# Optimization experiments

Measured on AMD Instinct MI355X. Metric: run time of the kernel, lower is better.

## Reference

```python
import jax, jax.numpy as jnp
import numpy as np

B, T, L, H = 16, 16, 512, 768


def setup_inputs() -> dict:
    key = jax.random.key(0)
    k1, k2, k3, k4, k5, k6 = jax.random.split(key, 6)
    hn = jax.random.normal(k1, (B, L, H), dtype=jnp.float32)
    decoder_out = jax.random.normal(k2, (B, L, H), dtype=jnp.float32)
    W1 = jax.random.normal(k3, (H, H), dtype=jnp.float32) * (1.0 / np.sqrt(H))
    W2 = jax.random.normal(k4, (H, H), dtype=jnp.float32) * (1.0 / np.sqrt(H))
    V = jax.random.normal(k5, (H,), dtype=jnp.float32) * (1.0 / np.sqrt(H))
    # Ragged, consistent pointer indices: T monotone segment starts per sample,
    # gold boundary Yindex[b,t] in [Xindex[b,t], L).
    step = L // T  # 32
    Xindex = jnp.broadcast_to(jnp.arange(T, dtype=jnp.int64) * step, (B, T))
    offsets = jax.random.randint(k6, (B, T), 0, step, dtype=jnp.int64)
    Yindex = Xindex + offsets
    lens = jnp.full((B,), L, dtype=jnp.int64)
    return {"hn": hn, "decoder_out": decoder_out, "W1": W1, "W2": W2, "V": V,
            "Xindex": Xindex, "Yindex": Yindex, "lens": lens}


def reference(hn, decoder_out, W1, W2, V, Xindex, Yindex, lens):
    # Faithful batched form of training_decoder + pointerLayer:
    #   for each sample i, step j:
    #     en = hn[i, Xindex[i,j]:lens[i]]            (ragged suffix)
    #     dj = decoder_out[i, Yindex[i,j]]           (cur_dj = decoder_out[cur_groundy])
    #     s  = selu(V @ selu(W1 en + W2 dj))
    #     loss += NLL(log_softmax(s), Yindex[i,j]-Xindex[i,j])
    WE = jnp.einsum('blh,gh->blg', hn, W1)                        # [B,L,H]  nnW1(en)
    dj = jnp.take_along_axis(decoder_out, Yindex[:, :, None], axis=1)  # [B,T,H]
    WD = jnp.einsum('bth,gh->btg', dj, W2)                        # [B,T,H]  nnW2(dj)
    act = jax.nn.selu(WE[:, None, :, :] + WD[:, :, None, :])      # [B,T,L,H]
    scores = jax.nn.selu(jnp.einsum('btlh,h->btl', act, V))       # [B,T,L]
    pos = jnp.arange(hn.shape[1])
    mask = (pos[None, None, :] >= Xindex[:, :, None]) & (pos[None, None, :] < lens[:, None, None])
    neg_inf = jnp.finfo(scores.dtype).min
    masked = jnp.where(mask, scores, neg_inf)
    logp = masked - jax.scipy.special.logsumexp(masked, axis=-1, keepdims=True)
    # logits index (Yindex - Xindex) in the sliced array == global index Yindex
    gold = jnp.take_along_axis(logp, Yindex[:, :, None], axis=-1)[..., 0]  # [B,T]
    return -jnp.mean(gold)
```

## Files before the change

### kernel.cpp

```cpp
#include <hip/hip_runtime.h>
#include <hip/hip_bf16.h>
#include <math.h>

#define SELU_SCALE 1.0507009873554805f
#define SELU_ALPHA 1.6732632423543772f

static constexpr int B_ = 16, T_ = 16, L_ = 512, H_ = 768;

typedef __bf16 bf16x8 __attribute__((ext_vector_type(8)));
typedef __bf16 bf16x4 __attribute__((ext_vector_type(4)));
typedef float  f32x4  __attribute__((ext_vector_type(4)));

__device__ __forceinline__ float bf_lo(unsigned u) { return __uint_as_float(u << 16); }
__device__ __forceinline__ float bf_hi(unsigned u) { return __uint_as_float(u & 0xFFFF0000u); }

__device__ __forceinline__ float selu_core(float x) {
    float e = fmaf(__expf(x), SELU_ALPHA, -SELU_ALPHA);
    return x > 0.0f ? x : e;
}

__device__ __forceinline__ bf16x4 cvt4(float4 f) {
    bf16x4 o;
    o.x = (__bf16)f.x; o.y = (__bf16)f.y; o.z = (__bf16)f.z; o.w = (__bf16)f.w;
    return o;
}

__global__ __launch_bounds__(256) void prep_k(
        const float* __restrict__ hn, const float* __restrict__ w1,
        const float* __restrict__ w2, const float* __restrict__ dec,
        const int* __restrict__ Yi,
        __bf16* __restrict__ hnb, __bf16* __restrict__ w1b,
        __bf16* __restrict__ w2b, __bf16* __restrict__ djb) {
    const int N0 = B_ * L_ * H_ / 4;
    const int NW = H_ * H_ / 4;
    const int N1 = N0 + NW, N2 = N1 + NW;
    int i = blockIdx.x * 256 + threadIdx.x;
    if (i < N0) {
        ((bf16x4*)hnb)[i] = cvt4(((const float4*)hn)[i]);
    } else if (i < N1) {
        int j = i - N0;
        ((bf16x4*)w1b)[j] = cvt4(((const float4*)w1)[j]);
    } else if (i < N2) {
        int j = i - N1;
        ((bf16x4*)w2b)[j] = cvt4(((const float4*)w2)[j]);
    } else {
        int j = i - N2;
        int bt = j / 192, c = j % 192;
        int b = bt >> 4;
        int y = Yi[bt];
        ((bf16x4*)djb)[bt * 192 + c] =
            cvt4(((const float4*)dec)[(b * L_ + y) * 192 + c]);
    }
}

__device__ __forceinline__ void load16_lds(const __bf16* g, __bf16* l) {
    __builtin_amdgcn_global_load_lds(
        (const __attribute__((address_space(1))) unsigned int*)g,
        (__attribute__((address_space(3))) unsigned int*)l, 16, 0, 0);
}
__device__ __forceinline__ int sw3(int row) { return (row ^ (row >> 2)) & 3; }

__global__ __launch_bounds__(256) void gemm_k(
        const __bf16* __restrict__ hnb, const __bf16* __restrict__ djb,
        const __bf16* __restrict__ w1b, const __bf16* __restrict__ w2b,
        __bf16* __restrict__ web, __bf16* __restrict__ wdb) {
    __shared__ __bf16 As[64 * 32];
    __shared__ __bf16 Bs[128 * 32];

    int bx = blockIdx.x;
    const __bf16* A; const __bf16* Bw; __bf16* C;
    if (bx < 768) { A = hnb; Bw = w1b; C = web; }
    else          { bx -= 768; A = djb; Bw = w2b; C = wdb; }
    const int m0 = (bx / 6) * 64, n0 = (bx % 6) * 128;

    const int wave = threadIdx.x >> 6;
    const int lane = threadIdx.x & 63;
    const int wm = (wave >> 1) * 32, wn = (wave & 1) * 64;
    const int lr = lane & 15, q = lane >> 4;

    const int arow = wave * 16 + (lane >> 2);
    const int acol = ((lane & 3) ^ sw3(arow)) * 8;
    const int brow0 = wave * 32 + (lane >> 2);
    const int bcol0 = ((lane & 3) ^ sw3(brow0)) * 8;
    const int brow1 = brow0 + 16;
    const int bcol1 = ((lane & 3) ^ sw3(brow1)) * 8;
    const __bf16* Ag  = A  + (size_t)(m0 + arow)  * 768 + acol;
    const __bf16* Bg0 = Bw + (size_t)(n0 + brow0) * 768 + bcol0;
    const __bf16* Bg1 = Bw + (size_t)(n0 + brow1) * 768 + bcol1;
    __bf16* Asw = &As[wave * 16 * 32];
    __bf16* Bsw0 = &Bs[wave * 32 * 32];
    __bf16* Bsw1 = Bsw0 + 16 * 32;

    int aoff[2], boff[4];
#pragma unroll
    for (int i = 0; i < 2; ++i) {
        int r = wm + i * 16 + lr;
        aoff[i] = r * 32 + ((q ^ sw3(r)) & 3) * 8;
    }
#pragma unroll
    for (int j = 0; j < 4; ++j) {
        int r = wn + j * 16 + lr;
        boff[j] = r * 32 + ((q ^ sw3(r)) & 3) * 8;
    }

    f32x4 acc[2][4] = {};

    for (int k0 = 0; k0 < 768; k0 += 32) {
        load16_lds(Ag  + k0, Asw);
        load16_lds(Bg0 + k0, Bsw0);
        load16_lds(Bg1 + k0, Bsw1);
        __syncthreads();
        bf16x8 af[2], bfr[4];
#pragma unroll
        for (int i = 0; i < 2; ++i) af[i]  = *(const bf16x8*)&As[aoff[i]];
#pragma unroll
        for (int j = 0; j < 4; ++j) bfr[j] = *(const bf16x8*)&Bs[boff[j]];
#pragma unroll
        for (int i = 0; i < 2; ++i)
#pragma unroll
            for (int j = 0; j < 4; ++j)
                acc[i][j] = __builtin_amdgcn_mfma_f32_16x16x32_bf16(af[i], bfr[j], acc[i][j], 0, 0, 0);
        __syncthreads();
    }

#pragma unroll
    for (int i = 0; i < 2; ++i)
#pragma unroll
        for (int j = 0; j < 4; ++j)
#pragma unroll
            for (int r = 0; r < 4; ++r) {
                int row = m0 + wm + i * 16 + q * 4 + r;
                int col = n0 + wn + j * 16 + lr;
                C[(size_t)row * 768 + col] = (__bf16)acc[i][j][r];
            }
}

__global__ __launch_bounds__(256) void scores_k(
        const __bf16* __restrict__ web, const __bf16* __restrict__ wdb,
        const float* __restrict__ V, const int* __restrict__ Xi,
        float* __restrict__ scores) {
    __shared__ float    we_s[16][772];
    __shared__ unsigned wd_s[16][388];
    __shared__ float    v_s[768];

    const int b = blockIdx.x, l0 = blockIdx.y * 16;

    for (int c = threadIdx.x; c < 16 * 96; c += 256) {
        int r = c / 96, cc = c % 96;
        uint4 v = *(const uint4*)(web + ((size_t)(b * L_ + l0 + r)) * H_ + cc * 8);
        float4 f0, f1;
        f0.x = bf_lo(v.x); f0.y = bf_hi(v.x); f0.z = bf_lo(v.y); f0.w = bf_hi(v.y);
        f1.x = bf_lo(v.z); f1.y = bf_hi(v.z); f1.z = bf_lo(v.w); f1.w = bf_hi(v.w);
        *(float4*)&we_s[r][cc * 8]     = f0;
        *(float4*)&we_s[r][cc * 8 + 4] = f1;
    }
    for (int c = threadIdx.x; c < 16 * 96; c += 256) {
        int r = c / 96, cc = c % 96;
        *(uint4*)&wd_s[r][cc * 4] = *(const uint4*)(wdb + ((size_t)(b * T_ + r)) * H_ + cc * 8);
    }
    if (threadIdx.x < 192) *(float4*)&v_s[threadIdx.x * 4] = ((const float4*)V)[threadIdx.x];
    __syncthreads();

    const int t = threadIdx.x >> 4;
    const int ls = threadIdx.x & 15;
    const int l = l0 + ls;
    const int X = Xi[b * T_ + t];
    if (!__any(l >= X)) return;

    float a0 = 0.f, a1 = 0.f, a2 = 0.f, a3 = 0.f;
#pragma unroll 4
    for (int h = 0; h < H_; h += 8) {
        float4 w0 = *(const float4*)&we_s[ls][h];
        float4 w1 = *(const float4*)&we_s[ls][h + 4];
        uint4  wd = *(const uint4*)&wd_s[t][h >> 1];
        float4 v0 = *(const float4*)&v_s[h];
        float4 v1 = *(const float4*)&v_s[h + 4];
        a0 = fmaf(selu_core(w0.x + bf_lo(wd.x)), v0.x, a0);
        a1 = fmaf(selu_core(w0.y + bf_hi(wd.x)), v0.y, a1);
        a2 = fmaf(selu_core(w0.z + bf_lo(wd.y)), v0.z, a2);
        a3 = fmaf(selu_core(w0.w + bf_hi(wd.y)), v0.w, a3);
        a0 = fmaf(selu_core(w1.x + bf_lo(wd.z)), v1.x, a0);
        a1 = fmaf(selu_core(w1.y + bf_hi(wd.z)), v1.y, a1);
        a2 = fmaf(selu_core(w1.z + bf_lo(wd.w)), v1.z, a2);
        a3 = fmaf(selu_core(w1.w + bf_hi(wd.w)), v1.w, a3);
    }
    float dot = SELU_SCALE * ((a0 + a1) + (a2 + a3));
    float sc  = dot > 0.0f ? SELU_SCALE * dot
                           : SELU_SCALE * SELU_ALPHA * (__expf(dot) - 1.0f);
    scores[((size_t)(b * T_ + t)) * L_ + l] = sc;
}

__global__ __launch_bounds__(64) void loss_k(
        const float* __restrict__ scores, const int* __restrict__ Xi,
        const int* __restrict__ Yi, float* __restrict__ out) {
    const int bt = blockIdx.x;
    const int lane = threadIdx.x;
    const int X = Xi[bt];
    const int Y = Yi[bt];
    const float* row = scores + (size_t)bt * L_;

    float m = -INFINITY;
    for (int l = X + lane; l < L_; l += 64) m = fmaxf(m, row[l]);
#pragma unroll
    for (int off = 32; off > 0; off >>= 1) m = fmaxf(m, __shfl_xor(m, off));

    float s = 0.0f;
    for (int l = X + lane; l < L_; l += 64) s += expf(row[l] - m);
#pragma unroll
    for (int off = 32; off > 0; off >>= 1) s += __shfl_xor(s, off);

    if (lane == 0)
        atomicAdd(out, (m + logf(s) - row[Y]) * (1.0f / (B_ * T_)));
}

extern "C" void kernel_launch(void* const* d_in, const int* in_sizes, int n_in,
                              void* d_out, int out_size, void* d_ws, size_t ws_size,
                              hipStream_t stream) {
    const float* hn  = (const float*)d_in[0];
    const float* dec = (const float*)d_in[1];
    const float* W1  = (const float*)d_in[2];
    const float* W2  = (const float*)d_in[3];
    const float* V   = (const float*)d_in[4];
    const int*   Xi  = (const int*)d_in[5];
    const int*   Yi  = (const int*)d_in[6];
    float* out = (float*)d_out;

    char* ws = (char*)d_ws;
    size_t off = 0;
    auto alloc = [&](size_t bytes) -> char* {
        char* p = ws + off;
        off += (bytes + 255) & ~(size_t)255;
        return p;
    };
    __bf16* hnb    = (__bf16*)alloc((size_t)B_ * L_ * H_ * 2);
    __bf16* w1b    = (__bf16*)alloc((size_t)H_ * H_ * 2);
    __bf16* w2b    = (__bf16*)alloc((size_t)H_ * H_ * 2);
    __bf16* djb    = (__bf16*)alloc((size_t)B_ * T_ * H_ * 2);
    __bf16* web    = (__bf16*)alloc((size_t)B_ * L_ * H_ * 2);
    __bf16* wdb    = (__bf16*)alloc((size_t)B_ * T_ * H_ * 2);
    float*  scores = (float*)alloc((size_t)B_ * T_ * L_ * 4);

    hipMemsetAsync(out, 0, sizeof(float), stream);

    prep_k<<<7488, 256, 0, stream>>>(hn, W1, W2, dec, Yi, hnb, w1b, w2b, djb);

    gemm_k<<<792, 256, 0, stream>>>(hnb, djb, w1b, w2b, web, wdb);

    scores_k<<<dim3(B_, L_ / 16), 256, 0, stream>>>(web, wdb, V, Xi, scores);
    loss_k<<<B_ * T_, 64, 0, stream>>>(scores, Xi, Yi, out);
}
```

Before: 161.7 us.

## Fuse fp32-to-bf16 conversion of hn into GEMM A-tile load, widen K tile

Stops converting hn to bf16 in a separate prep pass. The GEMM now reads fp32 activations directly, converts them in registers and writes them to a swizzled LDS tile. The K step grows from 32 to 64 with a new XOR swizzle, the memset is folded into prep_k, and the loss kernel uses fast exp/log intrinsics. This removes a full write and re-read of a bf16 copy of hn, at the cost of reading A in fp32, which doubles A bandwidth in the GEMM. The synchronous register-path A loads also replace async LDS loads.

```diff
diff --git a/kernel.cpp b/kernel.cpp
--- a/kernel.cpp
+++ b/kernel.cpp
@@ -26,30 +26,24 @@
 }
 
 __global__ __launch_bounds__(256) void prep_k(
-        const float* __restrict__ hn, const float* __restrict__ w1,
-        const float* __restrict__ w2, const float* __restrict__ dec,
-        const int* __restrict__ Yi,
-        __bf16* __restrict__ hnb, __bf16* __restrict__ w1b,
-        __bf16* __restrict__ w2b, __bf16* __restrict__ djb) {
-    const int N0 = B_ * L_ * H_ / 4;
+        const float* __restrict__ w1, const float* __restrict__ w2,
+        const float* __restrict__ dec, const int* __restrict__ Yi,
+        __bf16* __restrict__ w1b, __bf16* __restrict__ w2b,
+        float* __restrict__ djf, float* __restrict__ out) {
     const int NW = H_ * H_ / 4;
-    const int N1 = N0 + NW, N2 = N1 + NW;
     int i = blockIdx.x * 256 + threadIdx.x;
-    if (i < N0) {
-        ((bf16x4*)hnb)[i] = cvt4(((const float4*)hn)[i]);
-    } else if (i < N1) {
-        int j = i - N0;
-        ((bf16x4*)w1b)[j] = cvt4(((const float4*)w1)[j]);
-    } else if (i < N2) {
-        int j = i - N1;
+    if (i == 0) out[0] = 0.0f;
+    if (i < NW) {
+        ((bf16x4*)w1b)[i] = cvt4(((const float4*)w1)[i]);
+    } else if (i < 2 * NW) {
+        int j = i - NW;
         ((bf16x4*)w2b)[j] = cvt4(((const float4*)w2)[j]);
     } else {
-        int j = i - N2;
+        int j = i - 2 * NW;
         int bt = j / 192, c = j % 192;
         int b = bt >> 4;
         int y = Yi[bt];
-        ((bf16x4*)djb)[bt * 192 + c] =
-            cvt4(((const float4*)dec)[(b * L_ + y) * 192 + c]);
+        ((float4*)djf)[bt * 192 + c] = ((const float4*)dec)[(b * L_ + y) * 192 + c];
     }
 }
 
@@ -58,19 +52,18 @@
         (const __attribute__((address_space(1))) unsigned int*)g,
         (__attribute__((address_space(3))) unsigned int*)l, 16, 0, 0);
 }
-__device__ __forceinline__ int sw3(int row) { return (row ^ (row >> 2)) & 3; }
 
 __global__ __launch_bounds__(256) void gemm_k(
-        const __bf16* __restrict__ hnb, const __bf16* __restrict__ djb,
+        const float* __restrict__ hn, const float* __restrict__ djf,
         const __bf16* __restrict__ w1b, const __bf16* __restrict__ w2b,
         __bf16* __restrict__ web, __bf16* __restrict__ wdb) {
-    __shared__ __bf16 As[64 * 32];
-    __shared__ __bf16 Bs[128 * 32];
+    __shared__ __bf16 As[64 * 64];
+    __shared__ __bf16 Bs[128 * 64];
 
     int bx = blockIdx.x;
-    const __bf16* A; const __bf16* Bw; __bf16* C;
-    if (bx < 768) { A = hnb; Bw = w1b; C = web; }
-    else          { bx -= 768; A = djb; Bw = w2b; C = wdb; }
+    const float* Af; const __bf16* Bw; __bf16* C;
+    if (bx < 768) { Af = hn; Bw = w1b; C = web; }
+    else          { bx -= 768; Af = djf; Bw = w2b; C = wdb; }
     const int m0 = (bx / 6) * 64, n0 = (bx % 6) * 128;
 
     const int wave = threadIdx.x >> 6;
@@ -78,48 +71,59 @@
     const int wm = (wave >> 1) * 32, wn = (wave & 1) * 64;
     const int lr = lane & 15, q = lane >> 4;
 
-    const int arow = wave * 16 + (lane >> 2);
-    const int acol = ((lane & 3) ^ sw3(arow)) * 8;
-    const int brow0 = wave * 32 + (lane >> 2);
-    const int bcol0 = ((lane & 3) ^ sw3(brow0)) * 8;
-    const int brow1 = brow0 + 16;
-    const int bcol1 = ((lane & 3) ^ sw3(brow1)) * 8;
-    const __bf16* Ag  = A  + (size_t)(m0 + arow)  * 768 + acol;
-    const __bf16* Bg0 = Bw + (size_t)(n0 + brow0) * 768 + bcol0;
-    const __bf16* Bg1 = Bw + (size_t)(n0 + brow1) * 768 + bcol1;
-    __bf16* Asw = &As[wave * 16 * 32];
-    __bf16* Bsw0 = &Bs[wave * 32 * 32];
-    __bf16* Bsw1 = Bsw0 + 16 * 32;
-
-    int aoff[2], boff[4];
-#pragma unroll
-    for (int i = 0; i < 2; ++i) {
-        int r = wm + i * 16 + lr;
-        aoff[i] = r * 32 + ((q ^ sw3(r)) & 3) * 8;
-    }
-#pragma unroll
-    for (int j = 0; j < 4; ++j) {
-        int r = wn + j * 16 + lr;
-        boff[j] = r * 32 + ((q ^ sw3(r)) & 3) * 8;
-    }
+    const int ar = threadIdx.x >> 2, asp = threadIdx.x & 3;
+    const int s0 = (asp * 2)     ^ (ar & 7);
+    const int s1 = (asp * 2 + 1) ^ (ar & 7);
+    const float* Ag = Af + (size_t)(m0 + ar) * 768 + asp * 16;
+    __bf16* Aw0 = &As[ar * 64 + s0 * 8];
+    __bf16* Aw1 = &As[ar * 64 + s1 * 8];
+
+    const int brow = wave * 8 + (lane >> 3);
+    const int bcol = ((lane & 7) ^ (lane >> 3)) * 8;
+    const __bf16* Bg = Bw + (size_t)(n0 + brow) * 768 + bcol;
+    __bf16* Bl = &Bs[(wave * 8) * 64];
+
+    int sl[2];
+    sl[0] = ((q)     ^ (lr & 7)) * 8;
+    sl[1] = ((4 + q) ^ (lr & 7)) * 8;
+    int arow_off[2], brow_off[4];
+#pragma unroll
+    for (int i = 0; i < 2; ++i) arow_off[i] = (wm + i * 16 + lr) * 64;
+#pragma unroll
+    for (int j = 0; j < 4; ++j) brow_off[j] = (wn + j * 16 + lr) * 64;
 
     f32x4 acc[2][4] = {};
 
-    for (int k0 = 0; k0 < 768; k0 += 32) {
-        load16_lds(Ag  + k0, Asw);
-        load16_lds(Bg0 + k0, Bsw0);
-        load16_lds(Bg1 + k0, Bsw1);
+    for (int k0 = 0; k0 < 768; k0 += 64) {
+#pragma unroll
+        for (int c = 0; c < 4; ++c)
+            load16_lds(Bg + (size_t)c * 32 * 768 + k0, Bl + c * 32 * 64);
+        float4 a0 = *(const float4*)(Ag + k0);
+        float4 a1 = *(const float4*)(Ag + k0 + 4);
+        float4 a2 = *(const float4*)(Ag + k0 + 8);
+        float4 a3 = *(const float4*)(Ag + k0 + 12);
+        bf16x8 p0, p1;
+        p0[0]=(__bf16)a0.x; p0[1]=(__bf16)a0.y; p0[2]=(__bf16)a0.z; p0[3]=(__bf16)a0.w;
+        p0[4]=(__bf16)a1.x; p0[5]=(__bf16)a1.y; p0[6]=(__bf16)a1.z; p0[7]=(__bf16)a1.w;
+        p1[0]=(__bf16)a2.x; p1[1]=(__bf16)a2.y; p1[2]=(__bf16)a2.z; p1[3]=(__bf16)a2.w;
+        p1[4]=(__bf16)a3.x; p1[5]=(__bf16)a3.y; p1[6]=(__bf16)a3.z; p1[7]=(__bf16)a3.w;
+        *(bf16x8*)Aw0 = p0;
+        *(bf16x8*)Aw1 = p1;
         __syncthreads();
-        bf16x8 af[2], bfr[4];
-#pragma unroll
-        for (int i = 0; i < 2; ++i) af[i]  = *(const bf16x8*)&As[aoff[i]];
-#pragma unroll
-        for (int j = 0; j < 4; ++j) bfr[j] = *(const bf16x8*)&Bs[boff[j]];
-#pragma unroll
-        for (int i = 0; i < 2; ++i)
-#pragma unroll
-            for (int j = 0; j < 4; ++j)
-                acc[i][j] = __builtin_amdgcn_mfma_f32_16x16x32_bf16(af[i], bfr[j], acc[i][j], 0, 0, 0);
+
+#pragma unroll
+        for (int kc = 0; kc < 2; ++kc) {
+            bf16x8 af[2], bfr[4];
+#pragma unroll
+            for (int i = 0; i < 2; ++i) af[i]  = *(const bf16x8*)&As[arow_off[i] + sl[kc]];
+#pragma unroll
+            for (int j = 0; j < 4; ++j) bfr[j] = *(const bf16x8*)&Bs[brow_off[j] + sl[kc]];
+#pragma unroll
+            for (int i = 0; i < 2; ++i)
+#pragma unroll
+                for (int j = 0; j < 4; ++j)
+                    acc[i][j] = __builtin_amdgcn_mfma_f32_16x16x32_bf16(af[i], bfr[j], acc[i][j], 0, 0, 0);
+        }
         __syncthreads();
     }
 
@@ -205,12 +209,12 @@
     for (int off = 32; off > 0; off >>= 1) m = fmaxf(m, __shfl_xor(m, off));
 
     float s = 0.0f;
-    for (int l = X + lane; l < L_; l += 64) s += expf(row[l] - m);
+    for (int l = X + lane; l < L_; l += 64) s += __expf(row[l] - m);
 #pragma unroll
     for (int off = 32; off > 0; off >>= 1) s += __shfl_xor(s, off);
 
     if (lane == 0)
-        atomicAdd(out, (m + logf(s) - row[Y]) * (1.0f / (B_ * T_)));
+        atomicAdd(out, (m + __logf(s) - row[Y]) * (1.0f / (B_ * T_)));
 }
 
 extern "C" void kernel_launch(void* const* d_in, const int* in_sizes, int n_in,
@@ -232,19 +236,16 @@
         off += (bytes + 255) & ~(size_t)255;
         return p;
     };
-    __bf16* hnb    = (__bf16*)alloc((size_t)B_ * L_ * H_ * 2);
     __bf16* w1b    = (__bf16*)alloc((size_t)H_ * H_ * 2);
     __bf16* w2b    = (__bf16*)alloc((size_t)H_ * H_ * 2);
-    __bf16* djb    = (__bf16*)alloc((size_t)B_ * T_ * H_ * 2);
+    float*  djf    = (float*)alloc((size_t)B_ * T_ * H_ * 4);
     __bf16* web    = (__bf16*)alloc((size_t)B_ * L_ * H_ * 2);
     __bf16* wdb    = (__bf16*)alloc((size_t)B_ * T_ * H_ * 2);
     float*  scores = (float*)alloc((size_t)B_ * T_ * L_ * 4);
 
-    hipMemsetAsync(out, 0, sizeof(float), stream);
-
-    prep_k<<<7488, 256, 0, stream>>>(hn, W1, W2, dec, Yi, hnb, w1b, w2b, djb);
-
-    gemm_k<<<792, 256, 0, stream>>>(hnb, djb, w1b, w2b, web, wdb);
+    prep_k<<<1344, 256, 0, stream>>>(W1, W2, dec, Yi, w1b, w2b, djf, out);
+
+    gemm_k<<<792, 256, 0, stream>>>(hn, djf, w1b, w2b, web, wdb);
 
     scores_k<<<dim3(B_, L_ / 16), 256, 0, stream>>>(web, wdb, V, Xi, scores);
     loss_k<<<B_ * T_, 64, 0, stream>>>(scores, Xi, Yi, out);
```

Result: no change. 163.6 us (+1.2%).
